# Kernel optimization log

Measured on AMD Instinct MI355X. Metric: run time of the kernel, lower is better.

Reference implementation:

```python
import jax, jax.numpy as jnp
import numpy as np

BATCH, N, D, N_STEPS = 16, 128, 128, 5
EPS = 1e-10

def setup_inputs() -> dict:
    key = jax.random.key(0)
    k1, k2 = jax.random.split(key)
    x = jax.random.normal(k1, (BATCH, D), dtype=jnp.float32)
    L = jax.random.normal(k2, (N, D, D), dtype=jnp.float32) * 0.1
    temperature = jnp.array(1.0, dtype=jnp.float32)
    target_similarity = jnp.array(-0.5, dtype=jnp.float32)
    step_size = jnp.array(0.1, dtype=jnp.float32)
    return {"x": x, "L": L, "temperature": temperature,
            "target_similarity": target_similarity, "step_size": step_size}

def _bases(L):
    # Cayley transform per bubble: U = (I + A)^{-1} (I - A), A skew-symmetric
    A = L - jnp.swapaxes(L, -1, -2)               # [N, d, d]
    I = jnp.eye(L.shape[-1], dtype=L.dtype)
    return jnp.linalg.solve(I[None] + A, I[None] - A)  # [N, d, d]

def reference(x, L, temperature, target_similarity, step_size):
    n = L.shape[0]
    bases = _bases(L)                              # [N, d, d]

    # measurements[b, i] = x[b] @ U_i
    measurements = jnp.einsum('bd,ndk->bnk', x, bases)  # [B, N, d]

    # surface tension: pairwise Frobenius distance between bases
    diff_b = bases[None, :] - bases[:, None]       # [N, N, d, d]
    tension = jnp.sqrt(jnp.sum(diff_b ** 2, axis=(-2, -1)) + 1e-8)  # [N, N]

    temp = jnp.maximum(jnp.abs(temperature), 0.01)
    interaction = jax.nn.softmax(-tension / temp, axis=-1)  # [N, N]
    mask = 1.0 - jnp.eye(n, dtype=x.dtype)
    w = (mask * interaction)[None]                 # [1, N, N]
    step = jnp.clip(jnp.abs(step_size), 0.001, 0.5)

    state = measurements
    for _ in range(N_STEPS):
        state_n = state / (jnp.linalg.norm(state, axis=-1, keepdims=True) + EPS)
        cos_sim = jnp.einsum('bnd,bmd->bnm', state_n, state_n)   # [B, N, N]
        force_mag = (cos_sim - target_similarity) * w            # [B, N, N]
        diff = state[:, :, None, :] - state[:, None, :, :]       # [B, N, N, d]
        diff_n = diff / (jnp.linalg.norm(diff, axis=-1, keepdims=True) + EPS)
        forces = jnp.einsum('bnm,bnmd->bnd', force_mag, diff_n)  # [B, N, d]
        state = state + step * forces
    equilibrium = state

    # expressions[b, i] = equilibrium[b, i] @ U_i^T
    expressions = jnp.einsum('bnd,nkd->bnk', equilibrium, bases)

    # density matrix per batch element
    m_norm = equilibrium / (jnp.linalg.norm(equilibrium, axis=-1, keepdims=True) + EPS)
    rho = jnp.einsum('bnd,bne->bde', m_norm, m_norm) / n         # [B, d, d]
    eigenvalues = jnp.linalg.eigvalsh(rho)                        # [B, d]
    eigenvalues = jnp.maximum(eigenvalues, 1e-12)
    output_dist = eigenvalues / jnp.sum(eigenvalues, axis=-1, keepdims=True)

    output_avg = jnp.mean(expressions, axis=1)                   # [B, d]
    return (output_avg, output_dist, rho, measurements, equilibrium,
            expressions, tension)
```

## Files before the change

kernel.cpp:

```cpp
#include <hip/hip_runtime.h>

#define EPSF 1e-10f

__device__ __forceinline__ float f4sel(float4 a, int cc) {
  float r = (cc == 0) ? a.x : a.y;
  r = (cc == 2) ? a.z : r;
  r = (cc == 3) ? a.w : r;
  return r;
}

__device__ __forceinline__ float dpp_quad_sum(float x) {
  x += __int_as_float(__builtin_amdgcn_update_dpp(
      0, __float_as_int(x), 0xB1, 0xf, 0xf, true));
  x += __int_as_float(__builtin_amdgcn_update_dpp(
      0, __float_as_int(x), 0x4E, 0xf, 0xf, true));
  return x;
}

__device__ __forceinline__ float dpp_red_sum64(float x) {
  x += __int_as_float(__builtin_amdgcn_update_dpp(0, __float_as_int(x), 0x111, 0xf, 0xf, true));
  x += __int_as_float(__builtin_amdgcn_update_dpp(0, __float_as_int(x), 0x112, 0xf, 0xf, true));
  x += __int_as_float(__builtin_amdgcn_update_dpp(0, __float_as_int(x), 0x114, 0xf, 0xe, true));
  x += __int_as_float(__builtin_amdgcn_update_dpp(0, __float_as_int(x), 0x118, 0xf, 0xc, true));
  x += __int_as_float(__builtin_amdgcn_update_dpp(0, __float_as_int(x), 0x142, 0xa, 0xf, true));
  x += __int_as_float(__builtin_amdgcn_update_dpp(0, __float_as_int(x), 0x143, 0xc, 0xf, true));
  return __int_as_float(__builtin_amdgcn_readlane(__float_as_int(x), 63));
}

#define SWZ4(i, j4) ((i) * 32 + ((j4) ^ ((i) & 31)))
#define SWZF(i, j) (SWZ4((i), (j) >> 2) * 4 + ((j) & 3))

__global__ __launch_bounds__(512, 2) void k_cayley(const float* __restrict__ L,
                                                   float* __restrict__ bases) {
  extern __shared__ float4 sm4[];
  float4* M4  = sm4;
  float*  Mf  = (float*)M4;
  float4* rb0 = sm4 + 4096;
  float4* rb1 = rb0 + 32;
  float*  cb0 = (float*)(rb1 + 32);
  float*  cb1 = cb0 + 128;
  const int n = blockIdx.x, t = threadIdx.x;
  const float* Ln = L + n * 16384;
  for (int f = t; f < 4096; f += 512) {
    int i = f >> 5, j4 = f & 31;
    M4[SWZ4(i, j4)] = ((const float4*)Ln)[f];
  }
  __syncthreads();
  for (int f = t; f < 16384; f += 512) {
    int i = f >> 7, j = f & 127;
    if (i < j) {
      int a = SWZF(i, j), b = SWZF(j, i);
      float va = Mf[a], vb = Mf[b];
      Mf[a] = va - vb;
      Mf[b] = vb - va;
    } else if (i == j) {
      Mf[SWZF(i, i)] = 1.0f;
    }
  }
  __syncthreads();
  const int i = t & 127;
  const int h2 = t >> 7;
  float4 Ar[8];
  #pragma unroll
  for (int u = 0; u < 8; ++u) Ar[u] = M4[SWZ4(i, h2 * 8 + u)];
  if (i == 0) {
    #pragma unroll
    for (int u = 0; u < 8; ++u) rb0[h2 * 8 + u] = Ar[u];
  }
  if (h2 == 0) cb0[i] = Ar[0].x;
  __syncthreads();
  for (int k = 0; k < 128; ++k) {
    const float4* rbC = (k & 1) ? rb1 : rb0;
    float4*       rbN = (k & 1) ? rb0 : rb1;
    const float*  cbC = (k & 1) ? cb1 : cb0;
    float*        cbN = (k & 1) ? cb0 : cb1;
    const float pivinv = 1.0f / cbC[k];
    const float coef = cbC[i] * pivinv;
    const int kj4 = k >> 2, kc = k & 3;
    const int nj4 = (k + 1) >> 2, ncc = (k + 1) & 3;
    const bool isPiv = (i == k);
    const bool isNext = (i == k + 1);
    float colv = 0.0f;
    #pragma unroll
    for (int u = 0; u < 8; ++u) {
      const int jj = h2 * 8 + u;
      float4 r = rbC[jj];
      float4 a;
      if (isPiv) {
        a.x = r.x * pivinv; a.y = r.y * pivinv;
        a.z = r.z * pivinv; a.w = r.w * pivinv;
        if (jj == kj4) {
          a.x = (kc == 0) ? pivinv : a.x;
          a.y = (kc == 1) ? pivinv : a.y;
          a.z = (kc == 2) ? pivinv : a.z;
          a.w = (kc == 3) ? pivinv : a.w;
        }
      } else {
        a = Ar[u];
        a.x -= coef * r.x; a.y -= coef * r.y;
        a.z -= coef * r.z; a.w -= coef * r.w;
        if (jj == kj4) {
          a.x = (kc == 0) ? -coef : a.x;
          a.y = (kc == 1) ? -coef : a.y;
          a.z = (kc == 2) ? -coef : a.z;
          a.w = (kc == 3) ? -coef : a.w;
        }
      }
      Ar[u] = a;
      if (jj == nj4) colv = f4sel(a, ncc);
      if (isNext) rbN[jj] = a;
    }
    if (h2 == (nj4 >> 3)) cbN[i] = colv;
    __syncthreads();
  }
  #pragma unroll
  for (int u = 0; u < 8; ++u) M4[SWZ4(i, h2 * 8 + u)] = Ar[u];
  __syncthreads();
  for (int f = t; f < 16384; f += 512) {
    int ii = f >> 7, j = f & 127;
    float v = Mf[SWZF(ii, j)];
    bases[n * 16384 + f] = 2.0f * v - ((ii == j) ? 1.0f : 0.0f);
  }
}

__global__ __launch_bounds__(256) void k_gramp(const float* __restrict__ bases,
                                               float* __restrict__ part) {
  __shared__ __align__(16) float tile[64][132];
  const int b = blockIdx.x, t = threadIdx.x;
  const int tx = t & 15, ty = t >> 4;
  const int i0 = tx * 8, j0 = ty * 8;
  const int k0 = b * 512;
  float acc[8][8];
  #pragma unroll
  for (int u = 0; u < 8; ++u)
    #pragma unroll
    for (int v = 0; v < 8; ++v) acc[u][v] = 0.f;
  for (int c0 = 0; c0 < 512; c0 += 64) {
    __syncthreads();
    for (int f = t; f < 8192; f += 256) {
      int i = f >> 6, kk = f & 63;
      tile[kk][i] = bases[i * 16384 + k0 + c0 + kk];
    }
    __syncthreads();
    for (int kk = 0; kk < 64; ++kk) {
      float4 a0 = *(const float4*)&tile[kk][i0];
      float4 a1 = *(const float4*)&tile[kk][i0 + 4];
      float4 b0 = *(const float4*)&tile[kk][j0];
      float4 b1 = *(const float4*)&tile[kk][j0 + 4];
      float av[8] = {a0.x, a0.y, a0.z, a0.w, a1.x, a1.y, a1.z, a1.w};
      float bv[8] = {b0.x, b0.y, b0.z, b0.w, b1.x, b1.y, b1.z, b1.w};
      #pragma unroll
      for (int u = 0; u < 8; ++u)
        #pragma unroll
        for (int v = 0; v < 8; ++v) acc[u][v] += av[u] * bv[v];
    }
  }
  float* P = part + b * 16384;
  #pragma unroll
  for (int u = 0; u < 8; ++u) {
    #pragma unroll
    for (int v4 = 0; v4 < 2; ++v4) {
      float4 o;
      o.x = acc[u][v4 * 4 + 0]; o.y = acc[u][v4 * 4 + 1];
      o.z = acc[u][v4 * 4 + 2]; o.w = acc[u][v4 * 4 + 3];
      *(float4*)&P[(i0 + u) * 128 + j0 + v4 * 4] = o;
    }
  }
}

__global__ __launch_bounds__(256) void k_gsum(const float* __restrict__ part,
                                              float* __restrict__ G) {
  const int g = blockIdx.x * 256 + threadIdx.x;
  float s = 0.f;
  for (int p = 0; p < 32; ++p) s += part[p * 16384 + g];
  G[g] = s;
}

__global__ __launch_bounds__(128) void k_wsoft(const float* __restrict__ G,
                                               const float* __restrict__ temp_p,
                                               float* __restrict__ w,
                                               float* __restrict__ tension_out) {
  const int i = blockIdx.x, t = threadIdx.x;
  __shared__ float rr[2], r2[2];
  float temp = fmaxf(fabsf(*temp_p), 0.01f);
  float gii = G[i * 128 + i], gjj = G[t * 128 + t], gij = G[i * 128 + t];
  float ten = sqrtf(fmaxf(gii + gjj - 2.0f * gij, 0.0f) + 1e-8f);
  tension_out[i * 128 + t] = ten;
  float logit = -ten / temp;
  float m = logit;
  for (int s = 32; s > 0; s >>= 1) m = fmaxf(m, __shfl_xor(m, s));
  if ((t & 63) == 0) rr[t >> 6] = m;
  __syncthreads();
  float mx = fmaxf(rr[0], rr[1]);
  float ex = expf(logit - mx);
  float ssum = ex;
  for (int s = 32; s > 0; s >>= 1) ssum += __shfl_xor(ssum, s);
  if ((t & 63) == 0) r2[t >> 6] = ssum;
  __syncthreads();
  float tot = r2[0] + r2[1];
  float wv = ex / tot;
  if (t == i) wv = 0.0f;
  w[i * 128 + t] = wv;
}

__global__ __launch_bounds__(128) void k_meas(const float* __restrict__ x,
                                              const float* __restrict__ bases,
                                              float* __restrict__ meas_out,
                                              float* __restrict__ state0,
                                              float* __restrict__ norms0) {
  const int n = blockIdx.x, t = threadIdx.x;
  __shared__ float xs[2048];
  __shared__ float red[2];
  for (int f = t; f < 2048; f += 128) xs[f] = x[f];
  __syncthreads();
  float acc[16];
  #pragma unroll
  for (int b = 0; b < 16; ++b) acc[b] = 0.f;
  for (int d = 0; d < 128; ++d) {
    float u = bases[n * 16384 + d * 128 + t];
    #pragma unroll
    for (int b = 0; b < 16; ++b) acc[b] += xs[b * 128 + d] * u;
  }
  for (int b = 0; b < 16; ++b) {
    meas_out[(b * 128 + n) * 128 + t] = acc[b];
    state0[(b * 128 + n) * 128 + t] = acc[b];
  }
  for (int b = 0; b < 16; ++b) {
    float v = acc[b] * acc[b];
    for (int s = 32; s > 0; s >>= 1) v += __shfl_down(v, s);
    if ((t & 63) == 0) red[t >> 6] = v;
    __syncthreads();
    if (t == 0) norms0[b * 128 + n] = sqrtf(red[0] + red[1]);
    __syncthreads();
  }
}

__global__ __launch_bounds__(128) void k_step(const float* __restrict__ src,
                                              float* __restrict__ dst,
                                              const float* __restrict__ w,
                                              const float* __restrict__ norms_in,
                                              float* __restrict__ norms_out,
                                              const float* __restrict__ tgt_p,
                                              const float* __restrict__ step_p) {
  const int b = blockIdx.x >> 7, n = blockIdx.x & 127, t = threadIdx.x;
  __shared__ float sn[128];
  __shared__ __align__(16) float chunk[32][132];
  __shared__ float red[2][32];
  __shared__ float cbuf[32];
  __shared__ float red2[2];
  const float target = *tgt_p;
  const float step = fminf(fmaxf(fabsf(*step_p), 0.001f), 0.5f);
  const float* srcb = src + b * 16384;
  float x_d = srcb[n * 128 + t];
  sn[t] = x_d;
  float norm_n = norms_in[b * 128 + n];
  float nn2 = norm_n * norm_n;
  float f_d = 0.0f;
  __syncthreads();
  for (int c0 = 0; c0 < 128; c0 += 32) {
    for (int f = t; f < 1024; f += 128) {
      int row = f >> 5, c4 = f & 31;
      ((float4*)&chunk[row][0])[c4] =
          ((const float4*)(srcb + (c0 + row) * 128))[c4];
    }
    __syncthreads();
    int m = t & 31, q = t >> 5;
    float dp = 0.f;
    const float* cr = &chunk[m][0];
    #pragma unroll
    for (int i2 = 0; i2 < 32; ++i2) {
      int dd = q * 32 + i2;
      dp += cr[dd] * sn[dd];
    }
    dp += __shfl_xor(dp, 32);
    int wave = t >> 6;
    if ((t & 63) < 32) red[wave][m] = dp;
    __syncthreads();
    if (t < 32) {
      float dot = red[0][t] + red[1][t];
      int mm = c0 + t;
      float norm_m = norms_in[b * 128 + mm];
      float sq = nn2 + norm_m * norm_m - 2.0f * dot;
      float wnm = w[n * 128 + mm];
      float cs = dot / ((norm_n + EPSF) * (norm_m + EPSF));
      float fm = (cs - target) * wnm;
      cbuf[t] = fm / (sqrtf(fmaxf(sq, 0.0f)) + EPSF);
    }
    __syncthreads();
    #pragma unroll
    for (int mi = 0; mi < 32; ++mi) f_d += cbuf[mi] * (x_d - chunk[mi][t]);
    __syncthreads();
  }
  float nv = x_d + step * f_d;
  dst[(b * 128 + n) * 128 + t] = nv;
  float v = nv * nv;
  for (int s = 32; s > 0; s >>= 1) v += __shfl_down(v, s);
  if ((t & 63) == 0) red2[t >> 6] = v;
  __syncthreads();
  if (t == 0) norms_out[b * 128 + n] = sqrtf(red2[0] + red2[1]);
}

__global__ __launch_bounds__(128) void k_expr(const float* __restrict__ eq,
                                              const float* __restrict__ bases,
                                              float* __restrict__ expr_out) {
  const int n = blockIdx.x, t = threadIdx.x;
  __shared__ __align__(16) float es[16][128];
  for (int f = t; f < 2048; f += 128)
    es[f >> 7][f & 127] = eq[((f >> 7) * 128 + n) * 128 + (f & 127)];
  __syncthreads();
  float acc[16];
  #pragma unroll
  for (int b = 0; b < 16; ++b) acc[b] = 0.f;
  const float4* U = (const float4*)(bases + n * 16384 + t * 128);
  for (int d4 = 0; d4 < 32; ++d4) {
    float4 u = U[d4];
    #pragma unroll
    for (int b = 0; b < 16; ++b) {
      float4 e4 = ((const float4*)&es[b][0])[d4];
      acc[b] += u.x * e4.x + u.y * e4.y + u.z * e4.z + u.w * e4.w;
    }
  }
  for (int b = 0; b < 16; ++b) expr_out[(b * 128 + n) * 128 + t] = acc[b];
}

__global__ __launch_bounds__(128) void k_avg(const float* __restrict__ expr,
                                             float* __restrict__ avg) {
  const int b = blockIdx.x, t = threadIdx.x;
  float s = 0.f;
  for (int n = 0; n < 128; ++n) s += expr[(b * 128 + n) * 128 + t];
  avg[b * 128 + t] = s * (1.0f / 128.0f);
}

__global__ __launch_bounds__(256) void k_rho(const float* __restrict__ eq,
                                             const float* __restrict__ norms,
                                             float* __restrict__ rho) {
  const int b = blockIdx.x >> 3, dt = blockIdx.x & 7;
  const int t = threadIdx.x;
  __shared__ float ch[32][129];
  int e = t & 127, dl = t >> 7;
  float acc[8];
  #pragma unroll
  for (int o = 0; o < 8; ++o) acc[o] = 0.f;
  for (int c0 = 0; c0 < 128; c0 += 32) {
    for (int f = t; f < 4096; f += 256) {
      int row = f >> 7, col = f & 127;
      int nn = c0 + row;
      float inv = 1.0f / (norms[b * 128 + nn] + EPSF);
      ch[row][col] = eq[(b * 128 + nn) * 128 + col] * inv;
    }
    __syncthreads();
    for (int nn = 0; nn < 32; ++nn) {
      float me = ch[nn][e];
      #pragma unroll
      for (int o = 0; o < 8; ++o) {
        int d = dt * 16 + dl + o * 2;
        acc[o] += ch[nn][d] * me;
      }
    }
    __syncthreads();
  }
  for (int o = 0; o < 8; ++o) {
    int d = dt * 16 + dl + o * 2;
    rho[(b * 128 + d) * 128 + e] = acc[o] * (1.0f / 128.0f);
  }
}

__global__ __launch_bounds__(512, 1) void k_tridiag(const float* __restrict__ rho,
                                                    float* __restrict__ dvec_g,
                                                    float* __restrict__ evec_g) {
  __shared__ __align__(16) float cb0[128];
  __shared__ __align__(16) float cb1[128];
  __shared__ __align__(16) float pbuf[128];
  __shared__ float dvl[128], evl[128];
  __shared__ float redS[8], redK[8], redX[1];
  const int bb = blockIdx.x, t = threadIdx.x;
  const int i = t >> 2, h = t & 3, wv = t >> 6;
  const float* R = rho + bb * 16384;
  float4 Ar[8];
  const float4* Rp = (const float4*)(R + i * 128 + h * 32);
  #pragma unroll
  for (int u = 0; u < 8; ++u) Ar[u] = Rp[u];
  if (h == 0) {
    cb0[i] = (i == 0) ? 0.f : Ar[0].x;
    if (i == 0) dvl[0] = Ar[0].x;
    if (i == 1) redX[0] = Ar[0].x;
  }
  {
    float s2w = dpp_red_sum64((h == 0 && i > 0) ? Ar[0].x * Ar[0].x : 0.f);
    if ((t & 63) == 0) redS[wv] = s2w;
  }
  __syncthreads();
  for (int k = 0; k < 126; ++k) {
    const float* cbC = (k & 1) ? cb1 : cb0;
    float*       cbN = (k & 1) ? cb0 : cb1;
    float sig2 = redS[0] + redS[1] + redS[2] + redS[3] +
                 redS[4] + redS[5] + redS[6] + redS[7];
    float x0 = redX[0];
    const bool skip = (sig2 < 1e-30f);
    float sig = sqrtf(sig2);
    float alpha = (x0 >= 0.f) ? -sig : sig;
    if (skip) alpha = 0.f;
    float beta = skip ? 0.f : 1.f / (sig2 - alpha * x0);
    float w0 = x0 - alpha;
    if (t == 0) evl[k] = alpha;
    const int jn4 = (k + 1) >> 2, ncc = (k + 1) & 3, hn = (k + 1) >> 5;
    float vt = (i == k + 1) ? w0 : cbC[i];
    const float4* cv4 = (const float4*)cbC;
    float pp = 0.f;
    #pragma unroll
    for (int u = 0; u < 8; ++u) {
      const int jj = h * 8 + u;
      float4 v = cv4[jj];
      if (jj == jn4) {
        v.x = (0 == ncc) ? w0 : v.x;
        v.y = (1 == ncc) ? w0 : v.y;
        v.z = (2 == ncc) ? w0 : v.z;
        v.w = (3 == ncc) ? w0 : v.w;
      }
      pp += Ar[u].x * v.x + Ar[u].y * v.y + Ar[u].z * v.z + Ar[u].w * v.w;
    }
    pp = dpp_quad_sum(pp);
    float p = beta * pp;
    if (i <= k) p = 0.f;
    if (h == 0) pbuf[i] = p;
    float kpw = dpp_red_sum64((h == 0) ? vt * p : 0.f);
    if ((t & 63) == 0) redK[wv] = kpw;
    __syncthreads();
    float K = (redK[0] + redK[1] + redK[2] + redK[3] +
               redK[4] + redK[5] + redK[6] + redK[7]) * beta * 0.5f;
    float cn = 0.f;
    if (i > k) {
      float qt = p - K * vt;
      const float4* pv4 = (const float4*)pbuf;
      #pragma unroll
      for (int u = 0; u < 8; ++u) {
        const int jj = h * 8 + u;
        float4 v = cv4[jj];
        if (jj == jn4) {
          v.x = (0 == ncc) ? w0 : v.x;
          v.y = (1 == ncc) ? w0 : v.y;
          v.z = (2 == ncc) ? w0 : v.z;
          v.w = (3 == ncc) ? w0 : v.w;
        }
        float4 pq = pv4[jj];
        float qx = pq.x - K * v.x, qy = pq.y - K * v.y;
        float qz = pq.z - K * v.z, qw = pq.w - K * v.w;
        Ar[u].x -= vt * qx + qt * v.x;
        Ar[u].y -= vt * qy + qt * v.y;
        Ar[u].z -= vt * qz + qt * v.z;
        Ar[u].w -= vt * qw + qt * v.w;
        if (jj == jn4) cn = f4sel(Ar[u], ncc);
      }
    }
    if (h == hn) cbN[i] = (i <= k + 1) ? 0.f : cn;
    if (i == k + 1 && h == hn) dvl[k + 1] = cn;
    if (i == k + 2 && h == hn) redX[0] = cn;
    float s2w = dpp_red_sum64((h == hn && i > k + 1) ? cn * cn : 0.f);
    if ((t & 63) == 0) redS[wv] = s2w;
    __syncthreads();
  }
  if (i == 126 && h == 3) dvl[126] = Ar[7].z;
  if (i == 127 && h == 3) { evl[126] = Ar[7].z; dvl[127] = Ar[7].w; }
  if (t == 0) evl[127] = 0.0f;
  __syncthreads();
  if (t < 128) {
    dvec_g[bb * 128 + t] = dvl[t];
    evec_g[bb * 128 + t] = evl[t];
  }
}

__global__ __launch_bounds__(1024, 1) void k_bisect(const float* __restrict__ dvec_g,
                                                    const float* __restrict__ evec_g,
                                                    float* __restrict__ lam_g) {
  const int bb = blockIdx.x >> 1, half = blockIdx.x & 1;
  const int t = threadIdx.x;
  const int idx = half * 64 + (t >> 4);
  const int c = t & 15;
  __shared__ __align__(8) float2 de[130];
  __shared__ float eabs_s[128];
  __shared__ float redlo[2], redhi[2];
  if (t < 128) {
    float d = dvec_g[bb * 128 + t];
    float e = evec_g[bb * 128 + t];
    de[t].x = d;
    de[t + 1].y = e * e;
    eabs_s[t] = fabsf(e);
    if (t == 0) {
      de[0].y = 0.f;
      de[128].x = 0.f;
      de[129] = make_float2(0.f, 0.f);
    }
  }
  __syncthreads();
  if (t < 128) {
    float d = de[t].x;
    float r = ((t > 0) ? eabs_s[t - 1] : 0.f) + ((t < 127) ? eabs_s[t] : 0.f);
    float lo_t = d - r, hi_t = d + r;
    for (int s = 32; s > 0; s >>= 1) {
      lo_t = fminf(lo_t, __shfl_xor(lo_t, s));
      hi_t = fmaxf(hi_t, __shfl_xor(hi_t, s));
    }
    if ((t & 63) == 0) { redlo[t >> 6] = lo_t; redhi[t >> 6] = hi_t; }
  }
  __syncthreads();
  float lo = fminf(redlo[0], redlo[1]);
  float hi = fmaxf(redhi[0], redhi[1]);
  const float frac = (float)(c + 1) * (1.0f / 17.0f);
  for (int it = 0; it < 8; ++it) {
    float mid = lo + (hi - lo) * frac;
    float q = de[0].x - mid;
    int cnt = (q < 0.0f) ? 1 : 0;
    float2 c0v = de[1], c1v = de[2];
    #pragma unroll 2
    for (int ii = 1; ii < 128; ++ii) {
      float2 nx = de[ii + 2];
      float denom = q;
      if (fabsf(denom) < 1e-25f) denom = (denom < 0.0f) ? -1e-25f : 1e-25f;
      q = (c0v.x - mid) - __fdividef(c0v.y, denom);
      cnt += (q < 0.0f) ? 1 : 0;
      c0v = c1v; c1v = nx;
    }
    bool isLo = (cnt <= idx);
    float cl = isLo ? mid : -1e30f;
    float ch = isLo ? 1e30f : mid;
    #pragma unroll
    for (int s = 1; s < 16; s <<= 1) {
      cl = fmaxf(cl, __shfl_xor(cl, s));
      ch = fminf(ch, __shfl_xor(ch, s));
    }
    lo = fmaxf(lo, cl);
    hi = fminf(hi, ch);
  }
  if (c == 0) lam_g[bb * 128 + idx] = 0.5f * (lo + hi);
}

__global__ __launch_bounds__(128) void k_dist(const float* __restrict__ lam_g,
                                              float* __restrict__ dist_out) {
  const int bb = blockIdx.x, t = threadIdx.x;
  __shared__ float rr[2];
  float evc = fmaxf(lam_g[bb * 128 + t], 1e-12f);
  float ssum = evc;
  for (int s = 32; s > 0; s >>= 1) ssum += __shfl_xor(ssum, s);
  if ((t & 63) == 0) rr[t >> 6] = ssum;
  __syncthreads();
  float tot = rr[0] + rr[1];
  dist_out[bb * 128 + t] = evc / tot;
}

extern "C" void kernel_launch(void* const* d_in, const int* in_sizes, int n_in,
                              void* d_out, int out_size, void* d_ws, size_t ws_size,
                              hipStream_t stream) {
  const float* x      = (const float*)d_in[0];
  const float* L      = (const float*)d_in[1];
  const float* temp_p = (const float*)d_in[2];
  const float* tgt_p  = (const float*)d_in[3];
  const float* step_p = (const float*)d_in[4];
  float* out = (float*)d_out;
  float* ws  = (float*)d_ws;

  float* bases = ws;
  float* G     = bases + 2097152;
  float* w     = G + 16384;
  float* s0    = w + 16384;
  float* s1    = s0 + 262144;
  float* n0    = s1 + 262144;
  float* n1    = n0 + 2048;
  float* dv    = n1 + 2048;
  float* ev    = dv + 2048;
  float* lamg  = ev + 2048;

  float* gpart = s0;

  float* o_avg  = out;
  float* o_dist = out + 2048;
  float* o_rho  = out + 4096;
  float* o_meas = out + 266240;
  float* o_eq   = out + 528384;
  float* o_expr = out + 790528;
  float* o_ten  = out + 1052672;

  hipFuncSetAttribute((const void*)k_cayley,
                      hipFuncAttributeMaxDynamicSharedMemorySize, 67584);

  k_cayley<<<128, 512, 67584, stream>>>(L, bases);
  k_gramp<<<32, 256, 0, stream>>>(bases, gpart);
  k_gsum<<<64, 256, 0, stream>>>(gpart, G);
  k_wsoft<<<128, 128, 0, stream>>>(G, temp_p, w, o_ten);
  k_meas<<<128, 128, 0, stream>>>(x, bases, o_meas, s0, n0);
  k_step<<<2048, 128, 0, stream>>>(s0, s1, w, n0, n1, tgt_p, step_p);
  k_step<<<2048, 128, 0, stream>>>(s1, s0, w, n1, n0, tgt_p, step_p);
  k_step<<<2048, 128, 0, stream>>>(s0, s1, w, n0, n1, tgt_p, step_p);
  k_step<<<2048, 128, 0, stream>>>(s1, s0, w, n1, n0, tgt_p, step_p);
  k_step<<<2048, 128, 0, stream>>>(s0, o_eq, w, n0, n1, tgt_p, step_p);
  k_expr<<<128, 128, 0, stream>>>(o_eq, bases, o_expr);
  k_avg<<<16, 128, 0, stream>>>(o_expr, o_avg);
  k_rho<<<128, 256, 0, stream>>>(o_eq, n1, o_rho);
  k_tridiag<<<16, 512, 0, stream>>>(o_rho, dv, ev);
  k_bisect<<<32, 1024, 0, stream>>>(dv, ev, lamg);
  k_dist<<<16, 128, 0, stream>>>(lamg, o_dist);
}
```

Baseline: 790.2 us.

## Stage whole batch state in swizzled LDS and factor force sum in k_step

Each k_step block now copies the full 128x128 state of its batch into dynamic LDS, using an XOR-swizzled float4 layout. It then computes all 128 dot products in one pass, replacing the four 32-row chunk iterations and their many barriers. The force accumulation is rewritten algebraically as csum*x - sum(c*s_m), which reads the state with float4-aligned swizzled accesses. The cost is about 66KB of LDS per block, which limits how many blocks can be resident per CU and leaves less room to overlap global-load latency.

```diff
diff --git a/kernel.cpp b/kernel.cpp
--- a/kernel.cpp
+++ b/kernel.cpp
@@ -235,6 +235,8 @@
   }
 }
 
+#define SSW(r, u) ((r) * 32 + ((u) ^ ((r) & 31)))
+
 __global__ __launch_bounds__(128) void k_step(const float* __restrict__ src,
                                               float* __restrict__ dst,
                                               const float* __restrict__ w,
@@ -242,56 +244,50 @@
                                               float* __restrict__ norms_out,
                                               const float* __restrict__ tgt_p,
                                               const float* __restrict__ step_p) {
+  extern __shared__ float sm[];
+  float4* S4  = (float4*)sm;
+  float*  Sf  = sm;
+  float*  cbuf = sm + 16384;
+  float*  red2 = cbuf + 128;
   const int b = blockIdx.x >> 7, n = blockIdx.x & 127, t = threadIdx.x;
-  __shared__ float sn[128];
-  __shared__ __align__(16) float chunk[32][132];
-  __shared__ float red[2][32];
-  __shared__ float cbuf[32];
-  __shared__ float red2[2];
   const float target = *tgt_p;
   const float step = fminf(fmaxf(fabsf(*step_p), 0.001f), 0.5f);
   const float* srcb = src + b * 16384;
-  float x_d = srcb[n * 128 + t];
-  sn[t] = x_d;
+  for (int f = t; f < 4096; f += 128) {
+    int r = f >> 5, u = f & 31;
+    S4[SSW(r, u)] = ((const float4*)srcb)[f];
+  }
+  __syncthreads();
+  float dp = 0.f;
+  #pragma unroll
+  for (int u = 0; u < 32; ++u) {
+    float4 a = S4[SSW(n, u)];
+    float4 m4 = S4[SSW(t, u)];
+    dp += a.x * m4.x + a.y * m4.y + a.z * m4.z + a.w * m4.w;
+  }
   float norm_n = norms_in[b * 128 + n];
-  float nn2 = norm_n * norm_n;
-  float f_d = 0.0f;
-  __syncthreads();
-  for (int c0 = 0; c0 < 128; c0 += 32) {
-    for (int f = t; f < 1024; f += 128) {
-      int row = f >> 5, c4 = f & 31;
-      ((float4*)&chunk[row][0])[c4] =
-          ((const float4*)(srcb + (c0 + row) * 128))[c4];
-    }
-    __syncthreads();
-    int m = t & 31, q = t >> 5;
-    float dp = 0.f;
-    const float* cr = &chunk[m][0];
-    #pragma unroll
-    for (int i2 = 0; i2 < 32; ++i2) {
-      int dd = q * 32 + i2;
-      dp += cr[dd] * sn[dd];
-    }
-    dp += __shfl_xor(dp, 32);
-    int wave = t >> 6;
-    if ((t & 63) < 32) red[wave][m] = dp;
-    __syncthreads();
-    if (t < 32) {
-      float dot = red[0][t] + red[1][t];
-      int mm = c0 + t;
-      float norm_m = norms_in[b * 128 + mm];
-      float sq = nn2 + norm_m * norm_m - 2.0f * dot;
-      float wnm = w[n * 128 + mm];
-      float cs = dot / ((norm_n + EPSF) * (norm_m + EPSF));
-      float fm = (cs - target) * wnm;
-      cbuf[t] = fm / (sqrtf(fmaxf(sq, 0.0f)) + EPSF);
-    }
-    __syncthreads();
-    #pragma unroll
-    for (int mi = 0; mi < 32; ++mi) f_d += cbuf[mi] * (x_d - chunk[mi][t]);
-    __syncthreads();
-  }
-  float nv = x_d + step * f_d;
+  float norm_m = norms_in[b * 128 + t];
+  float sq = norm_n * norm_n + norm_m * norm_m - 2.0f * dp;
+  float cs = dp / ((norm_n + EPSF) * (norm_m + EPSF));
+  float fm = (cs - target) * w[n * 128 + t];
+  cbuf[t] = fm / (sqrtf(fmaxf(sq, 0.0f)) + EPSF);
+  __syncthreads();
+  const int fq = t >> 2, fc = t & 3;
+  float x_d = Sf[SSW(n, fq) * 4 + fc];
+  float facc = 0.f, csum = 0.f;
+  const float4* c4 = (const float4*)cbuf;
+  #pragma unroll 4
+  for (int m4 = 0; m4 < 32; ++m4) {
+    float4 c = c4[m4];
+    int m0 = m4 * 4;
+    float s0v = Sf[SSW(m0 + 0, fq) * 4 + fc];
+    float s1v = Sf[SSW(m0 + 1, fq) * 4 + fc];
+    float s2v = Sf[SSW(m0 + 2, fq) * 4 + fc];
+    float s3v = Sf[SSW(m0 + 3, fq) * 4 + fc];
+    facc += c.x * s0v + c.y * s1v + c.z * s2v + c.w * s3v;
+    csum += (c.x + c.y) + (c.z + c.w);
+  }
+  float nv = x_d + step * (csum * x_d - facc);
   dst[(b * 128 + n) * 128 + t] = nv;
   float v = nv * nv;
   for (int s = 32; s > 0; s >>= 1) v += __shfl_down(v, s);
@@ -581,17 +577,19 @@
 
   hipFuncSetAttribute((const void*)k_cayley,
                       hipFuncAttributeMaxDynamicSharedMemorySize, 67584);
+  hipFuncSetAttribute((const void*)k_step,
+                      hipFuncAttributeMaxDynamicSharedMemorySize, 66064);
 
   k_cayley<<<128, 512, 67584, stream>>>(L, bases);
   k_gramp<<<32, 256, 0, stream>>>(bases, gpart);
   k_gsum<<<64, 256, 0, stream>>>(gpart, G);
   k_wsoft<<<128, 128, 0, stream>>>(G, temp_p, w, o_ten);
   k_meas<<<128, 128, 0, stream>>>(x, bases, o_meas, s0, n0);
-  k_step<<<2048, 128, 0, stream>>>(s0, s1, w, n0, n1, tgt_p, step_p);
-  k_step<<<2048, 128, 0, stream>>>(s1, s0, w, n1, n0, tgt_p, step_p);
-  k_step<<<2048, 128, 0, stream>>>(s0, s1, w, n0, n1, tgt_p, step_p);
-  k_step<<<2048, 128, 0, stream>>>(s1, s0, w, n1, n0, tgt_p, step_p);
-  k_step<<<2048, 128, 0, stream>>>(s0, o_eq, w, n0, n1, tgt_p, step_p);
+  k_step<<<2048, 128, 66064, stream>>>(s0, s1, w, n0, n1, tgt_p, step_p);
+  k_step<<<2048, 128, 66064, stream>>>(s1, s0, w, n1, n0, tgt_p, step_p);
+  k_step<<<2048, 128, 66064, stream>>>(s0, s1, w, n0, n1, tgt_p, step_p);
+  k_step<<<2048, 128, 66064, stream>>>(s1, s0, w, n1, n0, tgt_p, step_p);
+  k_step<<<2048, 128, 66064, stream>>>(s0, o_eq, w, n0, n1, tgt_p, step_p);
   k_expr<<<128, 128, 0, stream>>>(o_eq, bases, o_expr);
   k_avg<<<16, 128, 0, stream>>>(o_expr, o_avg);
   k_rho<<<128, 256, 0, stream>>>(o_eq, n1, o_rho);
```

Measured after the change: 980.7 us. 24.1% more time.
